# Optimization experiments

Measured on AMD Instinct MI355X. Metric: run time of the kernel, lower is better.

## Reference

```python
import jax, jax.numpy as jnp
import numpy as np

N_HEAD = 16

def setup_inputs() -> dict:
    key = jax.random.key(0)
    k1, k2, k3 = jax.random.split(key, 3)
    B, T, C = 4, 2048, 1024
    x = jax.random.normal(k1, (B, T, C), dtype=jnp.float32)
    W_qkv = jax.random.normal(k2, (3 * C, C), dtype=jnp.float32) * 0.02
    W_o = jax.random.normal(k3, (C, C), dtype=jnp.float32) * (0.02 / np.sqrt(2.0))
    return {"x": x, "W_qkv": W_qkv, "W_o": W_o}

def reference(x, W_qkv, W_o):
    B, T, C = x.shape
    H = N_HEAD
    d_k = C // H
    # combined qkv projection (torch Linear: y = x @ W^T)
    qkv = x @ W_qkv.T                      # (B, T, 3C)
    q, k, v = jnp.split(qkv, 3, axis=-1)
    def split_heads(t):
        return t.reshape(B, T, H, d_k).transpose(0, 2, 1, 3)  # (B, H, T, d_k)
    q, k, v = split_heads(q), split_heads(k), split_heads(v)
    scale = 1.0 / jnp.sqrt(jnp.asarray(d_k, dtype=x.dtype))
    scores = jnp.einsum('bhqd,bhkd->bhqk', q, k) * scale      # (B, H, T, T)
    causal = jnp.tril(jnp.ones((T, T), dtype=bool))           # True = keep
    scores = jnp.where(causal[None, None], scores, -jnp.inf)
    attn = jax.nn.softmax(scores, axis=-1)                    # no NaNs under causal mask
    out = jnp.einsum('bhqk,bhkd->bhqd', attn, v)              # (B, H, T, d_k)
    out = out.transpose(0, 2, 1, 3).reshape(B, T, C)
    return out @ W_o.T
```

## Files before the change

kernel.cpp:

```cpp
#include <hip/hip_runtime.h>
#include <hip/hip_bf16.h>
#include <cstdint>

typedef __bf16 bf16;
typedef __bf16 bf16x8 __attribute__((ext_vector_type(8)));
typedef float f32x4 __attribute__((ext_vector_type(4)));

#define MFMA16(A, B, C) __builtin_amdgcn_mfma_f32_16x16x32_bf16((A), (B), (C), 0, 0, 0)

__device__ __forceinline__ void async16(const bf16* g, bf16* l) {
    __builtin_amdgcn_global_load_lds(
        (const __attribute__((address_space(1))) void*)g,
        (__attribute__((address_space(3))) void*)l, 16, 0, 0);
}

__global__ void cvt_all(const float* __restrict__ x, const float* __restrict__ wq,
                        const float* __restrict__ wo, bf16* __restrict__ xb,
                        bf16* __restrict__ wqb, bf16* __restrict__ wob) {
    const int bid = blockIdx.x;
    const float* s;
    bf16* d;
    int off;
    if (bid < 4096)      { s = x;  d = xb;  off = bid; }
    else if (bid < 5632) { s = wq; d = wqb; off = bid - 4096; }
    else                 { s = wo; d = wob; off = bid - 5632; }
    const size_t i = ((size_t)off * 256 + threadIdx.x) * 8;
    const float4 a = *(const float4*)(s + i);
    const float4 b2 = *(const float4*)(s + i + 4);
    bf16x8 r;
    r[0] = (bf16)a.x; r[1] = (bf16)a.y; r[2] = (bf16)a.z; r[3] = (bf16)a.w;
    r[4] = (bf16)b2.x; r[5] = (bf16)b2.y; r[6] = (bf16)b2.z; r[7] = (bf16)b2.w;
    *(bf16x8*)(d + i) = r;
}

template <int MODE>
__launch_bounds__(256, 3)
__global__ void gemm_nt(const bf16* __restrict__ A, const bf16* __restrict__ Bm,
                        void* __restrict__ O0, bf16* __restrict__ O1,
                        bf16* __restrict__ O2, int N, int K) {
    __shared__ alignas(16) bf16 As[128 * 64];
    __shared__ alignas(16) bf16 Bs[128 * 64];

    const int t = threadIdx.x;
    const int w = t >> 6, l = t & 63, quad = l >> 4, l15 = l & 15;
    const int wm = w & 1, wn = w >> 1;

    const int gx = (int)gridDim.x;
    const int nwg = gx * (int)gridDim.y;
    const int wg0 = (int)blockIdx.y * gx + (int)blockIdx.x;
    const int wg = (wg0 & 7) * (nwg >> 3) + (wg0 >> 3);
    const int m0 = (wg / gx) * 128, n0 = (wg % gx) * 128;

    f32x4 acc[4][4] = {};

    const int srow = t >> 3, sch = t & 7;
    const bf16* ga = A + (size_t)(m0 + srow) * K + sch * 8;
    const bf16* gb = Bm + (size_t)(n0 + srow) * K + sch * 8;

    for (int kt = 0; kt < K; kt += 64) {
        __syncthreads();
#pragma unroll
        for (int i = 0; i < 4; i++) {
            async16(ga + (size_t)i * 32 * K + kt, &As[(i * 256 + t) * 8]);
            async16(gb + (size_t)i * 32 * K + kt, &Bs[(i * 256 + t) * 8]);
        }
        __syncthreads();

#pragma unroll
        for (int s = 0; s < 2; s++) {
            bf16x8 af[4], bfr[4];
#pragma unroll
            for (int im = 0; im < 4; im++)
                af[im] = *(const bf16x8*)&As[(wm * 64 + im * 16 + l15) * 64 + s * 32 + quad * 8];
#pragma unroll
            for (int in = 0; in < 4; in++)
                bfr[in] = *(const bf16x8*)&Bs[(wn * 64 + in * 16 + l15) * 64 + s * 32 + quad * 8];
#pragma unroll
            for (int im = 0; im < 4; im++)
#pragma unroll
                for (int in = 0; in < 4; in++)
                    acc[im][in] = MFMA16(af[im], bfr[in], acc[im][in]);
        }
    }

    if (MODE == 0) {
        bf16* Q0 = (bf16*)O0;
#pragma unroll
        for (int in = 0; in < 4; in++) {
            const int n = n0 + wn * 64 + in * 16;
            const int sel = n >> 10;
            const int c = n & 1023;
            const int h = c >> 6;
            const int dd = c & 63;
            bf16* dst = (sel == 0) ? Q0 : ((sel == 1) ? O1 : O2);
#pragma unroll
            for (int im = 0; im < 4; im++) {
#pragma unroll
                for (int r = 0; r < 4; r++) {
                    const int m = m0 + wm * 64 + im * 16 + quad * 4 + r;
                    const int b = m >> 11, tt = m & 2047;
                    dst[((size_t)(b * 16 + h) * 2048 + tt) * 64 + dd + l15] =
                        (bf16)acc[im][in][r];
                }
            }
        }
    } else {
        float* Of = (float*)O0;
#pragma unroll
        for (int im = 0; im < 4; im++) {
#pragma unroll
            for (int in = 0; in < 4; in++) {
#pragma unroll
                for (int r = 0; r < 4; r++) {
                    const int m = m0 + wm * 64 + im * 16 + quad * 4 + r;
                    const int n = n0 + wn * 64 + in * 16 + l15;
                    Of[(size_t)m * N + n] = acc[im][in][r];
                }
            }
        }
    }
}

__launch_bounds__(256, 4)
__global__ void vtrans(const bf16* __restrict__ V, bf16* __restrict__ Vt) {
    __shared__ alignas(16) bf16 Ls[64 * 72];
    const int t = threadIdx.x, bh = blockIdx.y, tt = blockIdx.x;
#pragma unroll
    for (int i = 0; i < 2; i++) {
        const int id = i * 256 + t, r = id >> 3, c = id & 7;
        *(bf16x8*)&Ls[r * 72 + c * 8] =
            *(const bf16x8*)&V[((size_t)bh * 2048 + tt * 64 + r) * 64 + c * 8];
    }
    __syncthreads();
#pragma unroll
    for (int i = 0; i < 2; i++) {
        const int id = i * 256 + t, d = id >> 3, c = id & 7;
        bf16x8 v;
#pragma unroll
        for (int j = 0; j < 8; j++) v[j] = Ls[(c * 8 + j) * 72 + d];
        *(bf16x8*)&Vt[((size_t)bh * 64 + d) * 2048 + tt * 64 + c * 8] = v;
    }
}

__launch_bounds__(256, 4)
__global__ void attn_fwd(const bf16* __restrict__ Q, const bf16* __restrict__ Kk,
                         const bf16* __restrict__ Vt, bf16* __restrict__ O) {
    __shared__ alignas(16) bf16 Ks[64 * 72];
    __shared__ alignas(16) bf16 Vs[64 * 72];

    const int t = threadIdx.x, w = t >> 6, l = t & 63;
    const int quad = l >> 4, l15 = l & 15;
    const int bh = blockIdx.y, pair = blockIdx.x;
    const int b = bh >> 4, h = bh & 15;
    const int sr = t >> 3, sc = t & 7;

    const bf16* Qbase = Q + (size_t)bh * 2048 * 64;
    const bf16* Kbase = Kk + (size_t)bh * 2048 * 64;
    const bf16* Vbase = Vt + (size_t)bh * 64 * 2048;

    const int qt0 = pair, qt1 = 31 - pair;

    int kr[4];
#pragma unroll
    for (int nt = 0; nt < 4; nt++)
        kr[nt] = (nt >> 1) * 32 + (l15 >> 2) * 8 + (nt & 1) * 4 + (l15 & 3);

    bf16x8 aq[2][2];
#pragma unroll
    for (int hf = 0; hf < 2; hf++) {
        const int qrow = (hf ? qt1 : qt0) * 64 + w * 16 + l15;
        aq[hf][0] = *(const bf16x8*)&Qbase[(size_t)qrow * 64 + quad * 8];
        aq[hf][1] = *(const bf16x8*)&Qbase[(size_t)qrow * 64 + 32 + quad * 8];
#pragma unroll
        for (int j = 0; j < 8; j++) {
            aq[hf][0][j] = aq[hf][0][j] * (bf16)0.1803369f;
            aq[hf][1][j] = aq[hf][1][j] * (bf16)0.1803369f;
        }
    }

    bf16x8 ones;
#pragma unroll
    for (int j = 0; j < 8; j++) ones[j] = (bf16)1.0f;

    f32x4 liacc[2] = {};
    f32x4 oa[2][4] = {};

    bf16x8 rk0 = *(const bf16x8*)&Kbase[(size_t)sr * 64 + sc * 8];
    bf16x8 rk1 = *(const bf16x8*)&Kbase[(size_t)(sr + 32) * 64 + sc * 8];
    bf16x8 rv0 = *(const bf16x8*)&Vbase[(size_t)sr * 2048 + sc * 8];
    bf16x8 rv1 = *(const bf16x8*)&Vbase[(size_t)(sr + 32) * 2048 + sc * 8];

    for (int kt = 0; kt <= qt1; kt++) {
        __syncthreads();
        *(bf16x8*)&Ks[sr * 72 + sc * 8] = rk0;
        *(bf16x8*)&Ks[(sr + 32) * 72 + sc * 8] = rk1;
        *(bf16x8*)&Vs[sr * 72 + sc * 8] = rv0;
        *(bf16x8*)&Vs[(sr + 32) * 72 + sc * 8] = rv1;
        __syncthreads();

        if (kt < qt1) {
            const int kn = kt + 1;
            rk0 = *(const bf16x8*)&Kbase[(size_t)(kn * 64 + sr) * 64 + sc * 8];
            rk1 = *(const bf16x8*)&Kbase[(size_t)(kn * 64 + sr + 32) * 64 + sc * 8];
            rv0 = *(const bf16x8*)&Vbase[(size_t)sr * 2048 + kn * 64 + sc * 8];
            rv1 = *(const bf16x8*)&Vbase[(size_t)(sr + 32) * 2048 + kn * 64 + sc * 8];
        }

        const bool do0 = (kt <= qt0);

        bf16x8 ap[2][2];
#pragma unroll
        for (int np = 0; np < 2; np++) {
            bf16x8 ka[2][2];
#pragma unroll
            for (int i = 0; i < 2; i++) {
                ka[i][0] = *(const bf16x8*)&Ks[kr[2 * np + i] * 72 + quad * 8];
                ka[i][1] = *(const bf16x8*)&Ks[kr[2 * np + i] * 72 + 32 + quad * 8];
            }
#pragma unroll
            for (int hf = 0; hf < 2; hf++) {
                if (hf == 0 && !do0) continue;
                const bool diag = (kt == (hf ? qt1 : qt0));
#pragma unroll
                for (int i = 0; i < 2; i++) {
                    f32x4 s = {};
                    s = MFMA16(ka[i][0], aq[hf][0], s);
                    s = MFMA16(ka[i][1], aq[hf][1], s);
                    const int kbase = np * 32 + quad * 8 + i * 4;
#pragma unroll
                    for (int r = 0; r < 4; r++) {
                        float x = s[r];
                        if (diag && (kbase + r) > (w * 16 + l15)) x = -1e30f;
                        ap[hf][np][i * 4 + r] = (bf16)__builtin_amdgcn_exp2f(x);
                    }
                }
            }
        }

#pragma unroll
        for (int s2 = 0; s2 < 2; s2++) {
            if (do0) liacc[0] = MFMA16(ap[0][s2], ones, liacc[0]);
            liacc[1] = MFMA16(ap[1][s2], ones, liacc[1]);
#pragma unroll
            for (int dt = 0; dt < 4; dt++) {
                bf16x8 bv = *(const bf16x8*)&Vs[(dt * 16 + l15) * 72 + s2 * 32 + quad * 8];
                if (do0) oa[0][dt] = MFMA16(ap[0][s2], bv, oa[0][dt]);
                oa[1][dt] = MFMA16(ap[1][s2], bv, oa[1][dt]);
            }
        }
    }

#pragma unroll
    for (int hf = 0; hf < 2; hf++) {
        const int qt = hf ? qt1 : qt0;
#pragma unroll
        for (int r = 0; r < 4; r++) {
            const float inv = __builtin_amdgcn_rcpf(liacc[hf][r]);
            const int m = b * 2048 + qt * 64 + w * 16 + quad * 4 + r;
#pragma unroll
            for (int dt = 0; dt < 4; dt++) {
                O[(size_t)m * 1024 + h * 64 + dt * 16 + l15] = (bf16)(oa[hf][dt][r] * inv);
            }
        }
    }
}

extern "C" void kernel_launch(void* const* d_in, const int* in_sizes, int n_in,
                              void* d_out, int out_size, void* d_ws, size_t ws_size,
                              hipStream_t stream) {
    const float* x = (const float*)d_in[0];
    const float* wqkv = (const float*)d_in[1];
    const float* wo = (const float*)d_in[2];

    const size_t SZ = (size_t)8192 * 1024;
    bf16* xb = (bf16*)d_ws;
    bf16* wqb = xb + SZ;
    bf16* wob = wqb + (size_t)3072 * 1024;
    bf16* Qw = wob + (size_t)1024 * 1024;
    bf16* Kw = Qw + SZ;
    bf16* Vw = Kw + SZ;
    bf16* Vtw = xb;

    dim3 blk(256);
    cvt_all<<<6144, blk, 0, stream>>>(x, wqkv, wo, xb, wqb, wob);
    gemm_nt<0><<<dim3(24, 64), blk, 0, stream>>>(xb, wqb, Qw, Kw, Vw, 3072, 1024);
    vtrans<<<dim3(32, 64), blk, 0, stream>>>(Vw, Vtw);
    attn_fwd<<<dim3(16, 64), blk, 0, stream>>>(Qw, Kw, Vtw, Vw);
    gemm_nt<1><<<dim3(8, 64), blk, 0, stream>>>(Vw, wob, d_out, nullptr, nullptr, 1024, 1024);
}
```

Before: 244.2 us.

## Replace QKV projection GEMM with 256x256-tile 8-wave pingpong kernel

Adds a new GEMM kernel for the QKV projection that uses 256x256 output tiles, 512 threads (8 waves), double-buffered async global-to-LDS loads, and a barrier-interleaved schedule that splits the MFMA work into four phases with s_setprio around them, overlapping loads for the next k-tile with compute. Larger tiles raise arithmetic intensity and cut global/LDS traffic per FLOP compared with the previous 128x128 kernel. In exchange it uses much more LDS (128 KB per block) and more registers for the accumulators, which lowers occupancy. The grid shrinks to 384 blocks, which may leave parts of the device underused.

```diff
diff --git a/kernel.cpp b/kernel.cpp
--- a/kernel.cpp
+++ b/kernel.cpp
@@ -33,6 +33,172 @@
     *(bf16x8*)(d + i) = r;
 }
 
+__launch_bounds__(512, 2)
+__global__ void gemm8p(const bf16* __restrict__ A, const bf16* __restrict__ Bm,
+                       bf16* __restrict__ O0, bf16* __restrict__ O1,
+                       bf16* __restrict__ O2, int N, int K) {
+    __shared__ alignas(16) bf16 As[2 * 2 * 8192];
+    __shared__ alignas(16) bf16 Bs[2 * 2 * 8192];
+
+    const int t = threadIdx.x, w = t >> 6, l = t & 63;
+    const int quad = l >> 4, l15 = l & 15;
+    const int wm = w >> 2, wn = w & 3;
+    const int bh2 = wn >> 1;
+
+    const int nwg = (int)gridDim.x;
+    const int wg = ((int)blockIdx.x & 7) * (nwg >> 3) + ((int)blockIdx.x >> 3);
+    const int NBN = N >> 8;
+    const int m0 = (wg / NBN) * 256, n0 = (wg % NBN) * 256;
+
+    const int NT = K >> 6;
+
+    int a_src[2], b_src[2], sdst[2];
+#pragma unroll
+    for (int j = 0; j < 2; j++) {
+        const int id = j * 512 + t;
+        const int row = id >> 3, c = id & 7;
+        const int gco = (c ^ (row & 7)) << 3;
+        a_src[j] = (m0 + row) * K + gco;
+        b_src[j] = (n0 + row) * K + gco;
+        sdst[j] = id << 3;
+    }
+
+#define STAGE_A(kt_, buf, h)                                                  \
+    do {                                                                      \
+        async16(A + a_src[0] + (h) * 128 * K + (kt_) * 64,                    \
+                &As[(((buf) * 2 + (h)) << 13) + sdst[0]]);                    \
+        async16(A + a_src[1] + (h) * 128 * K + (kt_) * 64,                    \
+                &As[(((buf) * 2 + (h)) << 13) + sdst[1]]);                    \
+    } while (0)
+#define STAGE_B(kt_, buf, h)                                                  \
+    do {                                                                      \
+        async16(Bm + b_src[0] + (h) * 128 * K + (kt_) * 64,                   \
+                &Bs[(((buf) * 2 + (h)) << 13) + sdst[0]]);                    \
+        async16(Bm + b_src[1] + (h) * 128 * K + (kt_) * 64,                   \
+                &Bs[(((buf) * 2 + (h)) << 13) + sdst[1]]);                    \
+    } while (0)
+
+    const int sw = l15 & 7;
+    const int pcs0 = (quad ^ sw) << 3;
+    const int pcs1 = ((4 + quad) ^ sw) << 3;
+
+    f32x4 acc[8][4] = {};
+
+    STAGE_B(0, 0, 0); STAGE_B(0, 0, 1);
+    STAGE_A(0, 0, 0); STAGE_A(0, 0, 1);
+    STAGE_B(1, 1, 0); STAGE_B(1, 1, 1);
+    STAGE_A(1, 1, 0); STAGE_A(1, 1, 1);
+    asm volatile("s_waitcnt vmcnt(8)" ::: "memory");
+    __builtin_amdgcn_s_barrier();
+
+    for (int kt = 0; kt < NT; ++kt) {
+        const int cb = kt & 1;
+        const int kn = kt + 2;
+        const bool st = (kn < NT);
+        const int ab = ((cb * 2 + wm) << 13);
+        const int bb = ((cb * 2 + bh2) << 13);
+        const int brow = ((wn & 1) << 6) + l15;
+
+        bf16x8 af[4][2], bfr[4][2];
+
+#pragma unroll
+        for (int mf = 0; mf < 4; mf++) {
+            const int ro = ab + ((mf * 16 + l15) << 6);
+            af[mf][0] = *(const bf16x8*)&As[ro + pcs0];
+            af[mf][1] = *(const bf16x8*)&As[ro + pcs1];
+        }
+#pragma unroll
+        for (int nf = 0; nf < 4; nf++) {
+            const int ro = bb + ((brow + nf * 16) << 6);
+            bfr[nf][0] = *(const bf16x8*)&Bs[ro + pcs0];
+            bfr[nf][1] = *(const bf16x8*)&Bs[ro + pcs1];
+        }
+        asm volatile("" ::: "memory");
+        __builtin_amdgcn_s_barrier();
+        __builtin_amdgcn_s_setprio(1);
+#pragma unroll
+        for (int mf = 0; mf < 4; mf++)
+#pragma unroll
+            for (int nf = 0; nf < 2; nf++) {
+                acc[mf][nf] = MFMA16(af[mf][0], bfr[nf][0], acc[mf][nf]);
+                acc[mf][nf] = MFMA16(af[mf][1], bfr[nf][1], acc[mf][nf]);
+            }
+        __builtin_amdgcn_s_setprio(0);
+        __builtin_amdgcn_s_barrier();
+
+        if (st) { STAGE_B(kn, cb, 0); STAGE_B(kn, cb, 1); }
+        asm volatile("" ::: "memory");
+        __builtin_amdgcn_s_barrier();
+        __builtin_amdgcn_s_setprio(1);
+#pragma unroll
+        for (int mf = 0; mf < 4; mf++)
+#pragma unroll
+            for (int nf = 0; nf < 2; nf++) {
+                acc[mf][2 + nf] = MFMA16(af[mf][0], bfr[2 + nf][0], acc[mf][2 + nf]);
+                acc[mf][2 + nf] = MFMA16(af[mf][1], bfr[2 + nf][1], acc[mf][2 + nf]);
+            }
+        __builtin_amdgcn_s_setprio(0);
+        __builtin_amdgcn_s_barrier();
+
+#pragma unroll
+        for (int mf = 0; mf < 4; mf++) {
+            const int ro = ab + (((4 + mf) * 16 + l15) << 6);
+            af[mf][0] = *(const bf16x8*)&As[ro + pcs0];
+            af[mf][1] = *(const bf16x8*)&As[ro + pcs1];
+        }
+        asm volatile("" ::: "memory");
+        __builtin_amdgcn_s_barrier();
+        __builtin_amdgcn_s_setprio(1);
+#pragma unroll
+        for (int mf = 0; mf < 4; mf++)
+#pragma unroll
+            for (int nf = 0; nf < 2; nf++) {
+                acc[4 + mf][nf] = MFMA16(af[mf][0], bfr[nf][0], acc[4 + mf][nf]);
+                acc[4 + mf][nf] = MFMA16(af[mf][1], bfr[nf][1], acc[4 + mf][nf]);
+            }
+        __builtin_amdgcn_s_setprio(0);
+        __builtin_amdgcn_s_barrier();
+
+        if (st) { STAGE_A(kn, cb, 0); STAGE_A(kn, cb, 1); }
+        asm volatile("" ::: "memory");
+        __builtin_amdgcn_s_barrier();
+        __builtin_amdgcn_s_setprio(1);
+#pragma unroll
+        for (int mf = 0; mf < 4; mf++)
+#pragma unroll
+            for (int nf = 0; nf < 2; nf++) {
+                acc[4 + mf][2 + nf] = MFMA16(af[mf][0], bfr[2 + nf][0], acc[4 + mf][2 + nf]);
+                acc[4 + mf][2 + nf] = MFMA16(af[mf][1], bfr[2 + nf][1], acc[4 + mf][2 + nf]);
+            }
+        __builtin_amdgcn_s_setprio(0);
+        if (st) asm volatile("s_waitcnt vmcnt(8)" ::: "memory");
+        else    asm volatile("s_waitcnt vmcnt(0)" ::: "memory");
+        __builtin_amdgcn_s_barrier();
+    }
+
+#pragma unroll
+    for (int nf = 0; nf < 4; nf++) {
+        const int n = n0 + wn * 64 + nf * 16;
+        const int sel = n >> 10;
+        const int c = n & 1023;
+        const int h = c >> 6;
+        const int dd = c & 63;
+        bf16* dst = (sel == 0) ? O0 : ((sel == 1) ? O1 : O2);
+#pragma unroll
+        for (int mf = 0; mf < 8; mf++) {
+#pragma unroll
+            for (int r = 0; r < 4; r++) {
+                const int m = m0 + wm * 128 + mf * 16 + quad * 4 + r;
+                const int b = m >> 11, tt = m & 2047;
+                dst[((size_t)(b * 16 + h) * 2048 + tt) * 64 + dd + l15] =
+                    (bf16)acc[mf][nf][r];
+            }
+        }
+    }
+#undef STAGE_A
+#undef STAGE_B
+}
+
 template <int MODE>
 __launch_bounds__(256, 3)
 __global__ void gemm_nt(const bf16* __restrict__ A, const bf16* __restrict__ Bm,
@@ -283,7 +449,7 @@
 
     dim3 blk(256);
     cvt_all<<<6144, blk, 0, stream>>>(x, wqkv, wo, xb, wqb, wob);
-    gemm_nt<0><<<dim3(24, 64), blk, 0, stream>>>(xb, wqb, Qw, Kw, Vw, 3072, 1024);
+    gemm8p<<<dim3(384), dim3(512), 0, stream>>>(xb, wqb, Qw, Kw, Vw, 3072, 1024);
     vtrans<<<dim3(32, 64), blk, 0, stream>>>(Vw, Vtw);
     attn_fwd<<<dim3(16, 64), blk, 0, stream>>>(Qw, Kw, Vtw, Vw);
     gemm_nt<1><<<dim3(8, 64), blk, 0, stream>>>(Vw, wob, d_out, nullptr, nullptr, 1024, 1024);
```

Result: slower. 256.7 us (+5.1%).

## Fuse V transpose into QKV GEMM epilogue and swizzle K tile in LDS

Applied to the files above, without the earlier changes.

The QKV projection GEMM now writes the V third of its output directly in transposed (B,H,d,T) layout, staging the tile through swizzled shared memory. This removes the separate vtrans kernel and its extra read/write pass over V. The attention kernel's K tile in LDS is also stored with an XOR-style chunk rotation to reduce bank conflicts on the MFMA operand reads. The GEMM epilogue for V blocks gains two barriers and an LDS round trip, and buffers are remapped so the attention output reuses the bf16 x buffer.

```diff
diff --git a/kernel.cpp b/kernel.cpp
--- a/kernel.cpp
+++ b/kernel.cpp
@@ -38,8 +38,9 @@
 __global__ void gemm_nt(const bf16* __restrict__ A, const bf16* __restrict__ Bm,
                         void* __restrict__ O0, bf16* __restrict__ O1,
                         bf16* __restrict__ O2, int N, int K) {
-    __shared__ alignas(16) bf16 As[128 * 64];
-    __shared__ alignas(16) bf16 Bs[128 * 64];
+    __shared__ alignas(16) bf16 SM[2][128 * 64];
+    bf16* const As = SM[0];
+    bf16* const Bs = SM[1];
 
     const int t = threadIdx.x;
     const int w = t >> 6, l = t & 63, quad = l >> 4, l15 = l & 15;
@@ -84,23 +85,53 @@
     }
 
     if (MODE == 0) {
-        bf16* Q0 = (bf16*)O0;
-#pragma unroll
-        for (int in = 0; in < 4; in++) {
-            const int n = n0 + wn * 64 + in * 16;
-            const int sel = n >> 10;
-            const int c = n & 1023;
-            const int h = c >> 6;
-            const int dd = c & 63;
-            bf16* dst = (sel == 0) ? Q0 : ((sel == 1) ? O1 : O2);
-#pragma unroll
-            for (int im = 0; im < 4; im++) {
-#pragma unroll
-                for (int r = 0; r < 4; r++) {
-                    const int m = m0 + wm * 64 + im * 16 + quad * 4 + r;
-                    const int b = m >> 11, tt = m & 2047;
-                    dst[((size_t)(b * 16 + h) * 2048 + tt) * 64 + dd + l15] =
-                        (bf16)acc[im][in][r];
+        if (n0 >= 2048) {
+            __syncthreads();
+            bf16* const Ts = &SM[0][0];
+#pragma unroll
+            for (int in = 0; in < 4; in++) {
+                const int col = wn * 64 + in * 16 + l15;
+                const int cx = (col & 7) << 3;
+#pragma unroll
+                for (int im = 0; im < 4; im++) {
+                    const int row0 = (wm * 64 + im * 16 + quad * 4) ^ cx;
+#pragma unroll
+                    for (int r = 0; r < 4; r++)
+                        Ts[col * 128 + row0 + r] = (bf16)acc[im][in][r];
+                }
+            }
+            __syncthreads();
+            bf16* VtOut = O2;
+            const int bb = m0 >> 11, tt0 = m0 & 2047;
+            const int c0 = n0 - 2048;
+#pragma unroll
+            for (int p = 0; p < 8; p++) {
+                const int col = p * 16 + w * 4 + (l >> 4);
+                const int chunk = l & 15;
+                const int physc = ((chunk ^ (col & 7)) & 7) + (chunk & 8);
+                const bf16x8 v = *(const bf16x8*)&Ts[col * 128 + physc * 8];
+                const int cg = c0 + col, h = cg >> 6, d = cg & 63;
+                *(bf16x8*)&VtOut[((size_t)(bb * 16 + h) * 64 + d) * 2048 + tt0 + chunk * 8] = v;
+            }
+        } else {
+            bf16* Q0 = (bf16*)O0;
+#pragma unroll
+            for (int in = 0; in < 4; in++) {
+                const int n = n0 + wn * 64 + in * 16;
+                const int sel = n >> 10;
+                const int c = n & 1023;
+                const int h = c >> 6;
+                const int dd = c & 63;
+                bf16* dst = (sel == 0) ? Q0 : O1;
+#pragma unroll
+                for (int im = 0; im < 4; im++) {
+#pragma unroll
+                    for (int r = 0; r < 4; r++) {
+                        const int m = m0 + wm * 64 + im * 16 + quad * 4 + r;
+                        const int b = m >> 11, tt = m & 2047;
+                        dst[((size_t)(b * 16 + h) * 2048 + tt) * 64 + dd + l15] =
+                            (bf16)acc[im][in][r];
+                    }
                 }
             }
         }
@@ -122,27 +153,6 @@
 }
 
 __launch_bounds__(256, 4)
-__global__ void vtrans(const bf16* __restrict__ V, bf16* __restrict__ Vt) {
-    __shared__ alignas(16) bf16 Ls[64 * 72];
-    const int t = threadIdx.x, bh = blockIdx.y, tt = blockIdx.x;
-#pragma unroll
-    for (int i = 0; i < 2; i++) {
-        const int id = i * 256 + t, r = id >> 3, c = id & 7;
-        *(bf16x8*)&Ls[r * 72 + c * 8] =
-            *(const bf16x8*)&V[((size_t)bh * 2048 + tt * 64 + r) * 64 + c * 8];
-    }
-    __syncthreads();
-#pragma unroll
-    for (int i = 0; i < 2; i++) {
-        const int id = i * 256 + t, d = id >> 3, c = id & 7;
-        bf16x8 v;
-#pragma unroll
-        for (int j = 0; j < 8; j++) v[j] = Ls[(c * 8 + j) * 72 + d];
-        *(bf16x8*)&Vt[((size_t)bh * 64 + d) * 2048 + tt * 64 + c * 8] = v;
-    }
-}
-
-__launch_bounds__(256, 4)
 __global__ void attn_fwd(const bf16* __restrict__ Q, const bf16* __restrict__ Kk,
                          const bf16* __restrict__ Vt, bf16* __restrict__ O) {
     __shared__ alignas(16) bf16 Ks[64 * 72];
@@ -160,10 +170,15 @@
 
     const int qt0 = pair, qt1 = 31 - pair;
 
-    int kr[4];
-#pragma unroll
-    for (int nt = 0; nt < 4; nt++)
+    int kr[4], kchunk0[4], kchunk1[4];
+#pragma unroll
+    for (int nt = 0; nt < 4; nt++) {
         kr[nt] = (nt >> 1) * 32 + (l15 >> 2) * 8 + (nt & 1) * 4 + (l15 & 3);
+        const int g2 = 2 * (kr[nt] >> 3);
+        kchunk0[nt] = (quad + g2) & 7;
+        kchunk1[nt] = (4 + quad + g2) & 7;
+    }
+    const int scw = (sc + 2 * (sr >> 3)) & 7;
 
     bf16x8 aq[2][2];
 #pragma unroll
@@ -192,8 +207,8 @@
 
     for (int kt = 0; kt <= qt1; kt++) {
         __syncthreads();
-        *(bf16x8*)&Ks[sr * 72 + sc * 8] = rk0;
-        *(bf16x8*)&Ks[(sr + 32) * 72 + sc * 8] = rk1;
+        *(bf16x8*)&Ks[sr * 72 + scw * 8] = rk0;
+        *(bf16x8*)&Ks[(sr + 32) * 72 + scw * 8] = rk1;
         *(bf16x8*)&Vs[sr * 72 + sc * 8] = rv0;
         *(bf16x8*)&Vs[(sr + 32) * 72 + sc * 8] = rv1;
         __syncthreads();
@@ -214,8 +229,9 @@
             bf16x8 ka[2][2];
 #pragma unroll
             for (int i = 0; i < 2; i++) {
-                ka[i][0] = *(const bf16x8*)&Ks[kr[2 * np + i] * 72 + quad * 8];
-                ka[i][1] = *(const bf16x8*)&Ks[kr[2 * np + i] * 72 + 32 + quad * 8];
+                const int nt = 2 * np + i;
+                ka[i][0] = *(const bf16x8*)&Ks[kr[nt] * 72 + kchunk0[nt] * 8];
+                ka[i][1] = *(const bf16x8*)&Ks[kr[nt] * 72 + kchunk1[nt] * 8];
             }
 #pragma unroll
             for (int hf = 0; hf < 2; hf++) {
@@ -278,13 +294,11 @@
     bf16* wob = wqb + (size_t)3072 * 1024;
     bf16* Qw = wob + (size_t)1024 * 1024;
     bf16* Kw = Qw + SZ;
-    bf16* Vw = Kw + SZ;
-    bf16* Vtw = xb;
+    bf16* Vtw = Kw + SZ;
 
     dim3 blk(256);
     cvt_all<<<6144, blk, 0, stream>>>(x, wqkv, wo, xb, wqb, wob);
-    gemm_nt<0><<<dim3(24, 64), blk, 0, stream>>>(xb, wqb, Qw, Kw, Vw, 3072, 1024);
-    vtrans<<<dim3(32, 64), blk, 0, stream>>>(Vw, Vtw);
-    attn_fwd<<<dim3(16, 64), blk, 0, stream>>>(Qw, Kw, Vtw, Vw);
-    gemm_nt<1><<<dim3(8, 64), blk, 0, stream>>>(Vw, wob, d_out, nullptr, nullptr, 1024, 1024);
-}
+    gemm_nt<0><<<dim3(24, 64), blk, 0, stream>>>(xb, wqb, Qw, Kw, Vtw, 3072, 1024);
+    attn_fwd<<<dim3(16, 64), blk, 0, stream>>>(Qw, Kw, Vtw, xb);
+    gemm_nt<1><<<dim3(8, 64), blk, 0, stream>>>(xb, wob, d_out, nullptr, nullptr, 1024, 1024);
+}
```

Result: slower. 249.6 us (+2.2%).
